# Performance work log

Measured on AMD Instinct MI355X. Metric: run time of the kernel, lower is better.

Reference implementation:

```python
import jax, jax.numpy as jnp
import numpy as np

N = 100000      # nodes
E = 3200000     # edges
IN, HID, OUT = 512, 256, 16
K = 10
ALPHA = 0.1


def setup_inputs() -> dict:
    key = jax.random.key(0)
    k1, k2, k3, k4 = jax.random.split(key, 4)
    x = jax.random.normal(k1, (N, IN), dtype=jnp.float32)
    edge_index = jax.random.randint(k2, (2, E), 0, N, dtype=jnp.int64)
    # torch.nn.Linear weights are [out_features, in_features]
    W1 = jax.random.normal(k3, (HID, IN), dtype=jnp.float32) * (1.0 / np.sqrt(IN))
    b1 = jnp.zeros((HID,), dtype=jnp.float32)
    W2 = jax.random.normal(k4, (OUT, HID), dtype=jnp.float32) * (1.0 / np.sqrt(HID))
    b2 = jnp.zeros((OUT,), dtype=jnp.float32)
    return {"x": x, "edge_index": edge_index, "W1": W1, "b1": b1, "W2": W2, "b2": b2}


def reference(x, edge_index, W1, b1, W2, b2):
    # Eval mode: dropout(p=0.5) is identity.
    h = jax.nn.relu(x @ W1.T + b1)           # [N, HID]
    h = h @ W2.T + b2                        # [N, OUT]

    # GCN normalization with self loops (PyG gcn_norm, add_self_loops=True)
    loop = jnp.arange(N, dtype=edge_index.dtype)
    row = jnp.concatenate([edge_index[0], loop])   # source (x_j)
    col = jnp.concatenate([edge_index[1], loop])   # target (aggregate here)
    deg = jax.ops.segment_sum(jnp.ones(row.shape[0], dtype=h.dtype), col, num_segments=N)
    dinv = jnp.where(deg > 0, deg ** -0.5, 0.0)
    norm = dinv[row] * dinv[col]                   # [E+N]

    # APPNP: z_{k+1} = (1-alpha) * A_hat z_k + alpha * h
    def step(z, _):
        msg = norm[:, None] * z[row]                                   # [E+N, OUT]
        agg = jax.ops.segment_sum(msg, col, num_segments=N)            # [N, OUT]
        return (1.0 - ALPHA) * agg + ALPHA * h, None

    z, _ = jax.lax.scan(step, h, None, length=K)
    return jax.nn.log_softmax(z, axis=1)
```

## Files before the change

### kernel.cpp

```cpp
#include <hip/hip_runtime.h>
#include <hip/hip_bf16.h>

#define IN_F 512
#define HID_F 256
#define OUT_F 16
#define PHASE_DIV 12512
#define NXCD 8

typedef __bf16 bf8_t __attribute__((ext_vector_type(8)));
typedef float f4_t __attribute__((ext_vector_type(4)));
typedef unsigned short u16x4 __attribute__((ext_vector_type(4)));
typedef unsigned short u16x8 __attribute__((ext_vector_type(8)));

__device__ __forceinline__ unsigned short f2b(float f) {
  union { float f; unsigned u; } a; a.f = f;
  unsigned u = a.u;
  u += 0x7fffu + ((u >> 16) & 1u);
  return (unsigned short)(u >> 16);
}

__global__ void detect_k(const int* __restrict__ ei, int* __restrict__ flag) {
  if (threadIdx.x == 0 && blockIdx.x == 0) {
    int is64 = 1;
    for (int i = 0; i < 16; ++i)
      if (ei[2 * i + 1] != 0) is64 = 0;
    *flag = is64;
  }
}

__global__ void wcvt_k(const float* __restrict__ W1, const float* __restrict__ W2,
                       unsigned short* __restrict__ W1b, unsigned short* __restrict__ W2b) {
  int g = blockIdx.x * 256 + threadIdx.x;
  const int NW1 = (HID_F * IN_F) / 8;
  const int NW2 = (OUT_F * HID_F) / 8;
  if (g < NW1) {
    float4 v0 = ((const float4*)W1)[2 * g];
    float4 v1 = ((const float4*)W1)[2 * g + 1];
    u16x8 s = { f2b(v0.x), f2b(v0.y), f2b(v0.z), f2b(v0.w),
                f2b(v1.x), f2b(v1.y), f2b(v1.z), f2b(v1.w) };
    ((u16x8*)W1b)[g] = s;
  } else if (g < NW1 + NW2) {
    int q = g - NW1;
    float4 v0 = ((const float4*)W2)[2 * q];
    float4 v1 = ((const float4*)W2)[2 * q + 1];
    u16x8 s = { f2b(v0.x), f2b(v0.y), f2b(v0.z), f2b(v0.w),
                f2b(v1.x), f2b(v1.y), f2b(v1.z), f2b(v1.w) };
    ((u16x8*)W2b)[q] = s;
  }
}

__global__ void cvt_k(const int* __restrict__ ei, int* __restrict__ row32,
                      int* __restrict__ col32, int* __restrict__ cnt,
                      const int* __restrict__ flag, int E_) {
  int e = blockIdx.x * 256 + threadIdx.x;
  if (e >= E_) return;
  int r, c;
  if (*flag) {
    const long long* e64 = (const long long*)ei;
    r = (int)e64[e];
    c = (int)e64[E_ + e];
  } else {
    r = ei[e];
    c = ei[E_ + e];
  }
  row32[e] = r;
  col32[e] = c;
  atomicAdd(&cnt[c], 1);
}

__global__ void dinv_k(const int* __restrict__ cnt, float* __restrict__ dinv, int n) {
  int i = blockIdx.x * 256 + threadIdx.x;
  if (i < n) dinv[i] = rsqrtf((float)(cnt[i] + 1));
}

__global__ __launch_bounds__(256) void mlp_k(
    const float* __restrict__ x, const unsigned short* __restrict__ W1b,
    const float* __restrict__ b1, const unsigned short* __restrict__ W2b,
    const float* __restrict__ b2, const float* __restrict__ dinv,
    float* __restrict__ h, float* __restrict__ zs0, int n) {
  __shared__ unsigned short a_sh[64][72];
  __shared__ unsigned short hid_sh[64][264];
  __shared__ unsigned short w2_sh[16][264];
  int tid = threadIdx.x;
  int node0 = blockIdx.x * 64;
  int wvid = tid >> 6;
  int lane = tid & 63;
  int row16 = lane & 15;
  int kg = lane >> 4;

  {
    int r = tid >> 4;
    int c0 = (tid & 15) * 16;
    const u16x8* src = (const u16x8*)(W2b + r * HID_F + c0);
    *(u16x8*)&w2_sh[r][c0] = src[0];
    *(u16x8*)&w2_sh[r][c0 + 8] = src[1];
  }

  f4_t acc[4][4];
  #pragma unroll
  for (int mi = 0; mi < 4; ++mi)
    #pragma unroll
    for (int ni = 0; ni < 4; ++ni)
      acc[mi][ni] = (f4_t){0.f, 0.f, 0.f, 0.f};

  const unsigned short* wbase = W1b + (size_t)(wvid * 64 + row16) * IN_F + kg * 8;

  int arow = tid >> 2;
  int acol = (tid & 3) * 16;
  int anode = node0 + arow;
  const float* xrow = x + (size_t)anode * IN_F + acol;

  for (int kc = 0; kc < 8; ++kc) {
    int kb = kc * 64;
    __syncthreads();
    {
      float4 v0, v1, v2, v3;
      if (anode < n) {
        v0 = *(const float4*)(xrow + kb);
        v1 = *(const float4*)(xrow + kb + 4);
        v2 = *(const float4*)(xrow + kb + 8);
        v3 = *(const float4*)(xrow + kb + 12);
      } else {
        v0 = v1 = v2 = v3 = (float4){0.f, 0.f, 0.f, 0.f};
      }
      u16x8 s0 = { f2b(v0.x), f2b(v0.y), f2b(v0.z), f2b(v0.w),
                   f2b(v1.x), f2b(v1.y), f2b(v1.z), f2b(v1.w) };
      u16x8 s1 = { f2b(v2.x), f2b(v2.y), f2b(v2.z), f2b(v2.w),
                   f2b(v3.x), f2b(v3.y), f2b(v3.z), f2b(v3.w) };
      *(u16x8*)&a_sh[arow][acol] = s0;
      *(u16x8*)&a_sh[arow][acol + 8] = s1;
    }
    __syncthreads();
    #pragma unroll
    for (int ks = 0; ks < 2; ++ks) {
      bf8_t af[4], bfr[4];
      #pragma unroll
      for (int ni = 0; ni < 4; ++ni)
        bfr[ni] = *(const bf8_t*)(wbase + ni * 16 * IN_F + kb + ks * 32);
      #pragma unroll
      for (int mi = 0; mi < 4; ++mi)
        af[mi] = *(const bf8_t*)&a_sh[mi * 16 + row16][ks * 32 + kg * 8];
      #pragma unroll
      for (int mi = 0; mi < 4; ++mi)
        #pragma unroll
        for (int ni = 0; ni < 4; ++ni)
          acc[mi][ni] = __builtin_amdgcn_mfma_f32_16x16x32_bf16(bfr[ni], af[mi], acc[mi][ni], 0, 0, 0);
    }
  }
  __syncthreads();
  #pragma unroll
  for (int ni = 0; ni < 4; ++ni) {
    int hb = wvid * 64 + ni * 16 + kg * 4;
    float4 bias4 = *(const float4*)&b1[hb];
    #pragma unroll
    for (int mi = 0; mi < 4; ++mi) {
      int nl = mi * 16 + row16;
      float v0 = fmaxf(acc[mi][ni][0] + bias4.x, 0.f);
      float v1 = fmaxf(acc[mi][ni][1] + bias4.y, 0.f);
      float v2 = fmaxf(acc[mi][ni][2] + bias4.z, 0.f);
      float v3 = fmaxf(acc[mi][ni][3] + bias4.w, 0.f);
      u16x4 s = { f2b(v0), f2b(v1), f2b(v2), f2b(v3) };
      *(u16x4*)&hid_sh[nl][hb] = s;
    }
  }
  __syncthreads();
  f4_t acc2 = (f4_t){0.f, 0.f, 0.f, 0.f};
  #pragma unroll
  for (int kc = 0; kc < 8; ++kc) {
    bf8_t a2  = *(const bf8_t*)&hid_sh[wvid * 16 + row16][kc * 32 + kg * 8];
    bf8_t b2f = *(const bf8_t*)&w2_sh[row16][kc * 32 + kg * 8];
    acc2 = __builtin_amdgcn_mfma_f32_16x16x32_bf16(a2, b2f, acc2, 0, 0, 0);
  }
  float bias2 = b2[row16];
  #pragma unroll
  for (int r = 0; r < 4; ++r) {
    int nl = wvid * 16 + kg * 4 + r;
    int node = node0 + nl;
    if (node < n) {
      float v = acc2[r] + bias2;
      h[(size_t)node * OUT_F + row16] = v;
      zs0[(size_t)node * OUT_F + row16] = dinv[node] * v;
    }
  }
}

__global__ void scan_blocks(const int* __restrict__ cnt, int* __restrict__ offs,
                            int* __restrict__ bsum, int n) {
  __shared__ int wsum[4];
  int tid = threadIdx.x;
  int base = blockIdx.x * 1024 + tid * 4;
  int v0 = (base + 0 < n) ? cnt[base + 0] : 0;
  int v1 = (base + 1 < n) ? cnt[base + 1] : 0;
  int v2 = (base + 2 < n) ? cnt[base + 2] : 0;
  int v3 = (base + 3 < n) ? cnt[base + 3] : 0;
  int tsum = v0 + v1 + v2 + v3;
  int lane = tid & 63, wv = tid >> 6;
  int inc = tsum;
  #pragma unroll
  for (int off = 1; off < 64; off <<= 1) {
    int t = __shfl_up(inc, off, 64);
    if (lane >= off) inc += t;
  }
  if (lane == 63) wsum[wv] = inc;
  __syncthreads();
  int add = 0;
  #pragma unroll
  for (int j = 0; j < 4; ++j)
    if (j < wv) add += wsum[j];
  int ex = add + inc - tsum;
  if (base + 0 < n) offs[base + 0] = ex;
  if (base + 1 < n) offs[base + 1] = ex + v0;
  if (base + 2 < n) offs[base + 2] = ex + v0 + v1;
  if (base + 3 < n) offs[base + 3] = ex + v0 + v1 + v2;
  if (tid == 255) bsum[blockIdx.x] = add + inc;
}

__global__ void scan_top(int* __restrict__ bsum, int nb) {
  __shared__ int w0;
  int tid = threadIdx.x;
  int v = (tid < nb) ? bsum[tid] : 0;
  int inc = v;
  #pragma unroll
  for (int off = 1; off < 64; off <<= 1) {
    int t = __shfl_up(inc, off, 64);
    if ((tid & 63) >= off) inc += t;
  }
  if (tid == 63) w0 = inc;
  __syncthreads();
  int ex = inc - v + ((tid >= 64) ? w0 : 0);
  if (tid < nb) bsum[tid] = ex;
}

__global__ void scan_add(int* __restrict__ offs, const int* __restrict__ bsum,
                         int* __restrict__ cursor, int n) {
  int base = blockIdx.x * 1024 + threadIdx.x * 4;
  int b = bsum[blockIdx.x];
  #pragma unroll
  for (int j = 0; j < 4; ++j) {
    int i = base + j;
    if (i < n) { int v = offs[i] + b; offs[i] = v; cursor[i] = v; }
  }
}

__global__ __launch_bounds__(256) void scatter_x(
    const int* __restrict__ row32, const int* __restrict__ col32,
    int* __restrict__ cursor, int* __restrict__ nbr, int E_, int nph) {
  int grp = blockIdx.x & (NXCD - 1);
  int bid = blockIdx.x >> 3;
  int nbk = gridDim.x >> 3;
  int stride = nbk * 256;
  for (int p = grp; p < nph; p += NXCD) {
    for (int e = bid * 256 + threadIdx.x; e < E_; e += stride) {
      int c = col32[e];
      if (c / PHASE_DIV == p) {
        int pos = atomicAdd(&cursor[c], 1);
        nbr[pos] = row32[e];
      }
    }
  }
}

__global__ __launch_bounds__(256) void prop_k(
    const float* __restrict__ zs_in, float* __restrict__ zs_out,
    const float* __restrict__ h, const int* __restrict__ offs,
    const int* __restrict__ cnt, const int* __restrict__ nbr,
    const float* __restrict__ dinv, float* __restrict__ out, int fin, int n) {
  int tid = threadIdx.x;
  int node = blockIdx.x * 16 + (tid >> 4);
  int lane = tid & 15;
  if (node >= n) return;
  float di = dinv[node];
  int base = node * OUT_F + lane;
  float a0 = zs_in[base];
  float a1 = 0.f;
  int s = offs[node];
  int end = s + cnt[node];
  int e = s;
  for (; e + 4 <= end; e += 4) {
    int j0 = nbr[e], j1 = nbr[e + 1], j2 = nbr[e + 2], j3 = nbr[e + 3];
    a0 += zs_in[j0 * OUT_F + lane];
    a1 += zs_in[j1 * OUT_F + lane];
    a0 += zs_in[j2 * OUT_F + lane];
    a1 += zs_in[j3 * OUT_F + lane];
  }
  for (; e < end; ++e) a0 += zs_in[nbr[e] * OUT_F + lane];
  float z = 0.9f * di * (a0 + a1) + 0.1f * h[base];
  if (!fin) {
    zs_out[base] = di * z;
  } else {
    float m = z;
    #pragma unroll
    for (int sdx = 8; sdx; sdx >>= 1) m = fmaxf(m, __shfl_xor(m, sdx, 16));
    float ex = expf(z - m);
    float t = ex;
    #pragma unroll
    for (int sdx = 8; sdx; sdx >>= 1) t += __shfl_xor(t, sdx, 16);
    out[base] = z - m - logf(t);
  }
}

extern "C" void kernel_launch(void* const* d_in, const int* in_sizes, int n_in,
                              void* d_out, int out_size, void* d_ws, size_t ws_size,
                              hipStream_t stream) {
  const int Nn = in_sizes[0] / IN_F;
  const int Ee = in_sizes[1] / 2;
  const float* x  = (const float*)d_in[0];
  const int*   ei = (const int*)d_in[1];
  const float* W1 = (const float*)d_in[2];
  const float* b1 = (const float*)d_in[3];
  const float* W2 = (const float*)d_in[4];
  const float* b2 = (const float*)d_in[5];
  float* out = (float*)d_out;

  char* w = (char*)d_ws;
  auto alloc = [&](size_t bytes) {
    char* p = w;
    w += (bytes + 255) & ~(size_t)255;
    return p;
  };
  float* h      = (float*)alloc((size_t)Nn * OUT_F * 4);
  float* zsA    = (float*)alloc((size_t)Nn * OUT_F * 4);
  float* zsB    = (float*)alloc((size_t)Nn * OUT_F * 4);
  int*   cnt    = (int*)alloc((size_t)Nn * 4);
  float* dinv   = (float*)alloc((size_t)Nn * 4);
  int*   offs   = (int*)alloc((size_t)Nn * 4);
  int*   cursor = (int*)alloc((size_t)Nn * 4);
  int*   bsum   = (int*)alloc(1024);
  int*   flag   = (int*)alloc(256);
  int*   nbr    = (int*)alloc((size_t)Ee * 4);
  int*   col32  = (int*)alloc((size_t)Ee * 4);
  unsigned short* W1b = (unsigned short*)alloc((size_t)HID_F * IN_F * 2);
  unsigned short* W2b = (unsigned short*)alloc((size_t)OUT_F * HID_F * 2);
  int*   row32  = (int*)h;

  hipMemsetAsync(cnt, 0, (size_t)Nn * 4, stream);
  detect_k<<<1, 64, 0, stream>>>(ei, flag);
  wcvt_k<<<66, 256, 0, stream>>>(W1, W2, W1b, W2b);
  cvt_k<<<(Ee + 255) / 256, 256, 0, stream>>>(ei, row32, col32, cnt, flag, Ee);
  dinv_k<<<(Nn + 255) / 256, 256, 0, stream>>>(cnt, dinv, Nn);
  int nb = (Nn + 1023) / 1024;
  scan_blocks<<<nb, 256, 0, stream>>>(cnt, offs, bsum, Nn);
  scan_top<<<1, 128, 0, stream>>>(bsum, nb);
  scan_add<<<nb, 256, 0, stream>>>(offs, bsum, cursor, Nn);
  int nph = (Nn + PHASE_DIV - 1) / PHASE_DIV;
  scatter_x<<<1024, 256, 0, stream>>>(row32, col32, cursor, nbr, Ee, nph);
  mlp_k<<<(Nn + 63) / 64, 256, 0, stream>>>(x, W1b, b1, W2b, b2, dinv, h, zsA, Nn);

  for (int it = 0; it < 10; ++it) {
    const float* zin = (it & 1) ? zsB : zsA;
    float* zout = (it & 1) ? zsA : zsB;
    int fin = (it == 9) ? 1 : 0;
    prop_k<<<(Nn + 15) / 16, 256, 0, stream>>>(zin, zout, h, offs, cnt, nbr,
                                               dinv, out, fin, Nn);
  }
}
```

Before: 1.035 ms.

## Store propagation state in bf16 and widen the gather unroll

The scaled propagation vectors zs are now stored as bf16 instead of fp32. This halves the bytes each prop_k gather reads per neighbor and the bytes written per iteration. The neighbor loop is unrolled to 8 with four accumulators to keep more loads in flight, and scatter_x uses nontemporal loads and reads row only for edges that match the current phase. Rounding to bf16 over 10 iterations adds numerical error that may reach the tolerance limit.

```diff
diff --git a/kernel.cpp b/kernel.cpp
--- a/kernel.cpp
+++ b/kernel.cpp
@@ -17,6 +17,9 @@
   unsigned u = a.u;
   u += 0x7fffu + ((u >> 16) & 1u);
   return (unsigned short)(u >> 16);
+}
+__device__ __forceinline__ float b2f(unsigned short s) {
+  union { unsigned u; float f; } a; a.u = ((unsigned)s) << 16; return a.f;
 }
 
 __global__ void detect_k(const int* __restrict__ ei, int* __restrict__ flag) {
@@ -77,7 +80,7 @@
     const float* __restrict__ x, const unsigned short* __restrict__ W1b,
     const float* __restrict__ b1, const unsigned short* __restrict__ W2b,
     const float* __restrict__ b2, const float* __restrict__ dinv,
-    float* __restrict__ h, float* __restrict__ zs0, int n) {
+    float* __restrict__ h, unsigned short* __restrict__ zs0, int n) {
   __shared__ unsigned short a_sh[64][72];
   __shared__ unsigned short hid_sh[64][264];
   __shared__ unsigned short w2_sh[16][264];
@@ -179,7 +182,7 @@
     if (node < n) {
       float v = acc2[r] + bias2;
       h[(size_t)node * OUT_F + row16] = v;
-      zs0[(size_t)node * OUT_F + row16] = dinv[node] * v;
+      zs0[(size_t)node * OUT_F + row16] = f2b(dinv[node] * v);
     }
   }
 }
@@ -251,17 +254,18 @@
   int stride = nbk * 256;
   for (int p = grp; p < nph; p += NXCD) {
     for (int e = bid * 256 + threadIdx.x; e < E_; e += stride) {
-      int c = col32[e];
+      int c = __builtin_nontemporal_load(&col32[e]);
       if (c / PHASE_DIV == p) {
+        int r = __builtin_nontemporal_load(&row32[e]);
         int pos = atomicAdd(&cursor[c], 1);
-        nbr[pos] = row32[e];
+        nbr[pos] = r;
       }
     }
   }
 }
 
 __global__ __launch_bounds__(256) void prop_k(
-    const float* __restrict__ zs_in, float* __restrict__ zs_out,
+    const unsigned short* __restrict__ zs_in, unsigned short* __restrict__ zs_out,
     const float* __restrict__ h, const int* __restrict__ offs,
     const int* __restrict__ cnt, const int* __restrict__ nbr,
     const float* __restrict__ dinv, float* __restrict__ out, int fin, int n) {
@@ -271,22 +275,27 @@
   if (node >= n) return;
   float di = dinv[node];
   int base = node * OUT_F + lane;
-  float a0 = zs_in[base];
-  float a1 = 0.f;
+  float a0 = b2f(zs_in[base]);
+  float a1 = 0.f, a2 = 0.f, a3 = 0.f;
   int s = offs[node];
   int end = s + cnt[node];
   int e = s;
-  for (; e + 4 <= end; e += 4) {
+  for (; e + 8 <= end; e += 8) {
     int j0 = nbr[e], j1 = nbr[e + 1], j2 = nbr[e + 2], j3 = nbr[e + 3];
-    a0 += zs_in[j0 * OUT_F + lane];
-    a1 += zs_in[j1 * OUT_F + lane];
-    a0 += zs_in[j2 * OUT_F + lane];
-    a1 += zs_in[j3 * OUT_F + lane];
-  }
-  for (; e < end; ++e) a0 += zs_in[nbr[e] * OUT_F + lane];
-  float z = 0.9f * di * (a0 + a1) + 0.1f * h[base];
+    int j4 = nbr[e + 4], j5 = nbr[e + 5], j6 = nbr[e + 6], j7 = nbr[e + 7];
+    a0 += b2f(zs_in[j0 * OUT_F + lane]);
+    a1 += b2f(zs_in[j1 * OUT_F + lane]);
+    a2 += b2f(zs_in[j2 * OUT_F + lane]);
+    a3 += b2f(zs_in[j3 * OUT_F + lane]);
+    a0 += b2f(zs_in[j4 * OUT_F + lane]);
+    a1 += b2f(zs_in[j5 * OUT_F + lane]);
+    a2 += b2f(zs_in[j6 * OUT_F + lane]);
+    a3 += b2f(zs_in[j7 * OUT_F + lane]);
+  }
+  for (; e < end; ++e) a0 += b2f(zs_in[nbr[e] * OUT_F + lane]);
+  float z = 0.9f * di * ((a0 + a1) + (a2 + a3)) + 0.1f * h[base];
   if (!fin) {
-    zs_out[base] = di * z;
+    zs_out[base] = f2b(di * z);
   } else {
     float m = z;
     #pragma unroll
@@ -318,9 +327,9 @@
     w += (bytes + 255) & ~(size_t)255;
     return p;
   };
-  float* h      = (float*)alloc((size_t)Nn * OUT_F * 4);
-  float* zsA    = (float*)alloc((size_t)Nn * OUT_F * 4);
-  float* zsB    = (float*)alloc((size_t)Nn * OUT_F * 4);
+  float*          h   = (float*)alloc((size_t)Nn * OUT_F * 4);
+  unsigned short* zsA = (unsigned short*)alloc((size_t)Nn * OUT_F * 2);
+  unsigned short* zsB = (unsigned short*)alloc((size_t)Nn * OUT_F * 2);
   int*   cnt    = (int*)alloc((size_t)Nn * 4);
   float* dinv   = (float*)alloc((size_t)Nn * 4);
   int*   offs   = (int*)alloc((size_t)Nn * 4);
@@ -347,8 +356,8 @@
   mlp_k<<<(Nn + 63) / 64, 256, 0, stream>>>(x, W1b, b1, W2b, b2, dinv, h, zsA, Nn);
 
   for (int it = 0; it < 10; ++it) {
-    const float* zin = (it & 1) ? zsB : zsA;
-    float* zout = (it & 1) ? zsA : zsB;
+    const unsigned short* zin = (it & 1) ? zsB : zsA;
+    unsigned short* zout = (it & 1) ? zsA : zsB;
     int fin = (it == 9) ? 1 : 0;
     prop_k<<<(Nn + 15) / 16, 256, 0, stream>>>(zin, zout, h, offs, cnt, nbr,
                                                dinv, out, fin, Nn);
```

Measured after the change: 946.9 us. -8.5%, faster.
